# Performance work log

Hardware: AMD Instinct MI355X
Metric: run time of the kernel (lower is better)

The kernel has to match this reference:

```python
import jax, jax.numpy as jnp
import numpy as np

N_NODES = 50000
N_EDGES = 800000
NFEAT, NHID, NCLASS = 512, 64, 40


def setup_inputs() -> dict:
    key = jax.random.key(0)
    ks = jax.random.split(key, 10)
    x = jax.random.normal(ks[0], (N_NODES, NFEAT), dtype=jnp.float32)
    edge_weight = jax.random.uniform(ks[1], (N_EDGES,), dtype=jnp.float32)
    W1 = jax.random.normal(ks[2], (NFEAT, NHID), dtype=jnp.float32) / np.sqrt(NFEAT)
    b1 = jnp.zeros((NHID,), dtype=jnp.float32)
    W2 = jax.random.normal(ks[3], (NHID, NHID), dtype=jnp.float32) / np.sqrt(NHID)
    b2 = jnp.zeros((NHID,), dtype=jnp.float32)
    W3 = jax.random.normal(ks[4], (NHID, NCLASS), dtype=jnp.float32) / np.sqrt(NHID)
    b3 = jnp.zeros((NCLASS,), dtype=jnp.float32)
    row = jax.random.randint(ks[5], (N_EDGES,), 0, N_NODES, dtype=jnp.int32)
    col = jax.random.randint(ks[6], (N_EDGES,), 0, N_NODES, dtype=jnp.int32)
    return {"x": x, "edge_weight": edge_weight, "W1": W1, "b1": b1,
            "W2": W2, "b2": b2, "W3": W3, "b3": b3, "row": row, "col": col}


def _gcn_layer(h, W, b, row, col, ew):
    # support = h @ W + b ; out = spmm(adj, support)
    support = h @ W + b                      # [N, dout]
    msg = support[col] * ew[:, None]         # gather + scale, [E, dout]
    return jax.ops.segment_sum(msg, row, num_segments=N_NODES)


def reference(x, edge_weight, W1, b1, W2, b2, W3, b3, row, col):
    h = jax.nn.relu(_gcn_layer(x, W1, b1, row, col, edge_weight))
    # dropout: eval mode -> identity
    h = _gcn_layer(h, W2, b2, row, col, edge_weight)
    h = _gcn_layer(h, W3, b3, row, col, edge_weight)
    return jax.nn.log_softmax(h, axis=1)
```

## Files before the change

kernel.cpp:

```cpp
#include <hip/hip_runtime.h>
#include <hip/hip_bf16.h>

#define NNODES 50000
#define NEDGES 800000
#define NFEAT  512
#define NHID   64
#define NCLASS 40

#define CAP 48
#define CNTSTRIDE 16
#define EPT 4
#define FILL_CHUNKS ((NEDGES / EPT + 255) / 256)
#define GEMM1_BLOCKS ((NNODES + 31) / 32)
#define SPMM_BLOCKS ((NNODES + 15) / 16)

typedef __attribute__((ext_vector_type(8))) short short8;
typedef __attribute__((ext_vector_type(4))) float floatx4;

static __device__ __forceinline__ unsigned short f2bf(float f) {
    union { float f; unsigned u; } v; v.f = f;
    const unsigned r = v.u + 0x7fffu + ((v.u >> 16) & 1u);
    return (unsigned short)(r >> 16);
}
static __device__ __forceinline__ float bf2f(unsigned u) {
    union { unsigned u; float f; } v; v.u = u << 16;
    return v.f;
}

template<int NCB, int NVALID>
static __device__ __forceinline__ void convW_body(
    const float* __restrict__ W, unsigned short* __restrict__ wb, int idx) {
    const int lane = idx & 63;
    const int cb   = (idx >> 6) % NCB;
    const int kb   = idx / (64 * NCB);
    const int q = lane >> 4, m = lane & 15;
    const int c = cb * 16 + m;
    short8 v;
    #pragma unroll
    for (int j = 0; j < 8; ++j)
        v[j] = (c < NVALID)
             ? (short)f2bf(W[(size_t)(kb * 32 + q * 8 + j) * NVALID + c])
             : (short)0;
    *(short8*)(wb + (size_t)idx * 8) = v;
}

__global__ __launch_bounds__(256) void conv_kernel(
    const float* __restrict__ W1, unsigned short* __restrict__ wb1,
    const float* __restrict__ W2, unsigned short* __restrict__ wb2,
    const float* __restrict__ W3, unsigned short* __restrict__ wb3,
    int4* __restrict__ cnt4) {
    const int blk = blockIdx.x;
    const int tid = threadIdx.x;
    if (blk < 16) {
        convW_body<4, 64>(W1, wb1, blk * 256 + tid);
    } else if (blk < 18) {
        convW_body<4, 64>(W2, wb2, (blk - 16) * 256 + tid);
    } else if (blk < 20) {
        const int idx = (blk - 18) * 256 + tid;
        if (idx < 2 * 3 * 64) convW_body<3, 40>(W3, wb3, idx);
    } else {
        const int i = (blk - 20) * 256 + tid;
        if (i < NNODES * CNTSTRIDE / 4) cnt4[i] = make_int4(0, 0, 0, 0);
    }
}

__global__ __launch_bounds__(256) void bucket_gemm1_kernel(
    const int* __restrict__ row, const int* __restrict__ col,
    const float* __restrict__ ew, int* __restrict__ cnt,
    unsigned* __restrict__ bucket,
    const float* __restrict__ x, const unsigned short* __restrict__ wb,
    const float* __restrict__ b, unsigned short* __restrict__ outb) {
    const int blk  = blockIdx.x;
    const int tid  = threadIdx.x;
    const int base = blk / 3;
    const int r    = blk % 3;

    if (r == 2) {
        const int e = (base * 256 + tid) * EPT;
        if (e >= NEDGES) return;
        const int4   r4 = *(const int4*)(row + e);
        const int4   c4 = *(const int4*)(col + e);
        const float4 w4 = *(const float4*)(ew + e);
        const int p0 = atomicAdd(&cnt[r4.x * CNTSTRIDE], 1);
        const int p1 = atomicAdd(&cnt[r4.y * CNTSTRIDE], 1);
        const int p2 = atomicAdd(&cnt[r4.z * CNTSTRIDE], 1);
        const int p3 = atomicAdd(&cnt[r4.w * CNTSTRIDE], 1);
        if (p0 < CAP) bucket[(size_t)r4.x * CAP + p0] = (unsigned)c4.x | ((unsigned)f2bf(w4.x) << 16);
        if (p1 < CAP) bucket[(size_t)r4.y * CAP + p1] = (unsigned)c4.y | ((unsigned)f2bf(w4.y) << 16);
        if (p2 < CAP) bucket[(size_t)r4.z * CAP + p2] = (unsigned)c4.z | ((unsigned)f2bf(w4.z) << 16);
        if (p3 < CAP) bucket[(size_t)r4.w * CAP + p3] = (unsigned)c4.w | ((unsigned)f2bf(w4.w) << 16);
        return;
    }

    const int g = base * 2 + r;
    if (g >= GEMM1_BLOCKS) return;
    __shared__ float red[2][16][64];

    const int lane = tid & 63;
    const int wid  = tid >> 6;
    const int p  = wid >> 1;
    const int kh = wid & 1;
    const int q = lane >> 4, m = lane & 15;

    const int rowbase = g * 32 + p * 16;
    int rload = rowbase + m;
    if (rload >= NNODES) rload = NNODES - 1;
    const float* xp = x + (size_t)rload * NFEAT + kh * 256 + q * 8;

    floatx4 acc[4];
    #pragma unroll
    for (int cb = 0; cb < 4; ++cb) acc[cb] = (floatx4)0.f;

    #pragma unroll
    for (int kc = 0; kc < 2; ++kc) {
        float4 a0[4], a1[4];
        #pragma unroll
        for (int u = 0; u < 4; ++u) {
            a0[u] = *(const float4*)(xp + (kc * 4 + u) * 32);
            a1[u] = *(const float4*)(xp + (kc * 4 + u) * 32 + 4);
        }
        #pragma unroll
        for (int u = 0; u < 4; ++u) {
            short8 afrag;
            afrag[0] = (short)f2bf(a0[u].x); afrag[1] = (short)f2bf(a0[u].y);
            afrag[2] = (short)f2bf(a0[u].z); afrag[3] = (short)f2bf(a0[u].w);
            afrag[4] = (short)f2bf(a1[u].x); afrag[5] = (short)f2bf(a1[u].y);
            afrag[6] = (short)f2bf(a1[u].z); afrag[7] = (short)f2bf(a1[u].w);

            const int kbg = kh * 8 + kc * 4 + u;
            const unsigned short* wp = wb + ((size_t)(kbg * 4) * 64 + lane) * 8;
            #pragma unroll
            for (int cb = 0; cb < 4; ++cb) {
                const short8 bfrag = *(const short8*)(wp + (size_t)cb * 64 * 8);
                acc[cb] = __builtin_amdgcn_mfma_f32_16x16x32_bf16(
                    afrag, bfrag, acc[cb], 0, 0, 0);
            }
        }
    }

    if (kh == 1) {
        #pragma unroll
        for (int cb = 0; cb < 4; ++cb)
            #pragma unroll
            for (int i = 0; i < 4; ++i)
                red[p][q * 4 + i][cb * 16 + m] = acc[cb][i];
    }
    __syncthreads();
    if (kh == 1) return;

    const int orow = rowbase + q * 4;
    #pragma unroll
    for (int cb = 0; cb < 4; ++cb) {
        const int c = cb * 16 + m;
        const float bias = b[c];
        #pragma unroll
        for (int i = 0; i < 4; ++i) {
            const int rr2 = orow + i;
            if (rr2 < NNODES)
                outb[(size_t)rr2 * NHID + c] =
                    f2bf(acc[cb][i] + red[p][q * 4 + i][c] + bias);
        }
    }
}

template<bool RELU, int NCB, int NOUT>
__global__ __launch_bounds__(256) void spmm_gemm_kernel(
    const unsigned short* __restrict__ supb, const unsigned* __restrict__ bucket,
    const int* __restrict__ cnt, const unsigned short* __restrict__ wb,
    const float* __restrict__ bias, unsigned short* __restrict__ outb) {
    __shared__ unsigned ent[16][CAP];
    __shared__ unsigned short ht[16 * 72];

    const int tid  = threadIdx.x;
    const int wid  = tid >> 6;
    const int lane = tid & 63;
    const int half = lane >> 5;
    const int fp   = lane & 31;
    const int nb0  = blockIdx.x * 16;

    #pragma unroll
    for (int s = 0; s < 3; ++s) {
        const int idx = s * 256 + tid;
        const int ln  = idx / CAP;
        const int sl  = idx - ln * CAP;
        const int n   = nb0 + ln;
        int d = cnt[n * CNTSTRIDE];
        if (d > CAP) d = CAP;
        ent[ln][sl] = (sl < d) ? bucket[(size_t)n * CAP + sl] : 0u;
    }
    __syncthreads();

    const int lnb = wid * 4;
    float a0[4] = {0.f, 0.f, 0.f, 0.f}, a1[4] = {0.f, 0.f, 0.f, 0.f};
    int maxd = 0;
    #pragma unroll
    for (int jn = 0; jn < 4; ++jn) {
        int d = cnt[(nb0 + lnb + jn) * CNTSTRIDE];
        if (d > CAP) d = CAP;
        maxd = max(maxd, d);
    }

    for (int i = half; i < maxd; i += 8) {
        unsigned eb[4][4], vb[4][4];
        #pragma unroll
        for (int jn = 0; jn < 4; ++jn)
            #pragma unroll
            for (int j = 0; j < 4; ++j)
                eb[jn][j] = ent[lnb + jn][i + 2 * j];
        #pragma unroll
        for (int jn = 0; jn < 4; ++jn)
            #pragma unroll
            for (int j = 0; j < 4; ++j)
                vb[jn][j] = *(const unsigned*)(supb + (size_t)(eb[jn][j] & 0xffffu) * NHID + fp * 2);
        #pragma unroll
        for (int jn = 0; jn < 4; ++jn)
            #pragma unroll
            for (int j = 0; j < 4; ++j) {
                const float w = bf2f(eb[jn][j] >> 16);
                a0[jn] += w * bf2f(vb[jn][j] & 0xffffu);
                a1[jn] += w * bf2f(vb[jn][j] >> 16);
            }
    }
    #pragma unroll
    for (int jn = 0; jn < 4; ++jn) {
        a0[jn] += __shfl_xor(a0[jn], 32);
        a1[jn] += __shfl_xor(a1[jn], 32);
        if (RELU) { a0[jn] = fmaxf(a0[jn], 0.f); a1[jn] = fmaxf(a1[jn], 0.f); }
    }
    if (half == 0) {
        #pragma unroll
        for (int jn = 0; jn < 4; ++jn)
            *(unsigned*)&ht[(lnb + jn) * 72 + fp * 2] =
                (unsigned)f2bf(a0[jn]) | ((unsigned)f2bf(a1[jn]) << 16);
    }
    __syncthreads();

    if (wid != 0) return;
    const int q = lane >> 4, m = lane & 15;
    const unsigned short* hp = &ht[m * 72 + q * 8];

    floatx4 acc[NCB];
    #pragma unroll
    for (int cb = 0; cb < NCB; ++cb) acc[cb] = (floatx4)0.f;

    #pragma unroll
    for (int kb = 0; kb < 2; ++kb) {
        const short8 afrag = *(const short8*)(hp + kb * 32);
        const unsigned short* wp = wb + ((size_t)(kb * NCB) * 64 + lane) * 8;
        #pragma unroll
        for (int cb = 0; cb < NCB; ++cb) {
            const short8 bfrag = *(const short8*)(wp + (size_t)cb * 64 * 8);
            acc[cb] = __builtin_amdgcn_mfma_f32_16x16x32_bf16(
                afrag, bfrag, acc[cb], 0, 0, 0);
        }
    }

    const int rbase = nb0 + q * 4;
    #pragma unroll
    for (int cb = 0; cb < NCB; ++cb) {
        const int c = cb * 16 + m;
        if (c >= NOUT) continue;
        const float bv = bias[c];
        #pragma unroll
        for (int i = 0; i < 4; ++i)
            outb[(size_t)(rbase + i) * NOUT + c] = f2bf(acc[cb][i] + bv);
    }
}

__global__ __launch_bounds__(256) void spmm_bf40_lsm_kernel(
    const unsigned short* __restrict__ supb, const unsigned* __restrict__ bucket,
    const int* __restrict__ cnt, float* __restrict__ out) {
    __shared__ unsigned ent[16][CAP];

    const int tid = threadIdx.x;
    const int f   = tid & 63;
    const int wid = tid >> 6;
    const int nb0 = blockIdx.x * 16;

    #pragma unroll
    for (int s = 0; s < 3; ++s) {
        const int idx = s * 256 + tid;
        const int ln  = idx / CAP;
        const int sl  = idx - ln * CAP;
        const int n   = nb0 + ln;
        int d = cnt[n * CNTSTRIDE];
        if (d > CAP) d = CAP;
        ent[ln][sl] = (sl < d) ? bucket[(size_t)n * CAP + sl] : 0u;
    }
    __syncthreads();

    #pragma unroll
    for (int t = 0; t < 4; ++t) {
        const int ln = wid * 4 + t;
        const int n  = nb0 + ln;
        int deg = cnt[n * CNTSTRIDE];
        if (deg > CAP) deg = CAP;
        float acc = 0.f;
        if (f < NCLASS) {
            for (int i = 0; i < deg; i += 16) {
                unsigned eb[16]; float vb[16];
                #pragma unroll
                for (int j = 0; j < 16; ++j)
                    eb[j] = ent[ln][min(i + j, CAP - 1)];
                #pragma unroll
                for (int j = 0; j < 16; ++j)
                    vb[j] = bf2f(supb[(size_t)(eb[j] & 0xffffu) * NCLASS + f]);
                #pragma unroll
                for (int j = 0; j < 16; ++j)
                    acc += vb[j] * bf2f(eb[j] >> 16);
            }
        }
        float m = (f < NCLASS) ? acc : -1e30f;
        #pragma unroll
        for (int o = 32; o > 0; o >>= 1) m = fmaxf(m, __shfl_xor(m, o));
        float ex = (f < NCLASS) ? __expf(acc - m) : 0.f;
        #pragma unroll
        for (int o = 32; o > 0; o >>= 1) ex += __shfl_xor(ex, o);
        const float ls = __logf(ex) + m;
        if (f < NCLASS) out[(size_t)n * NCLASS + f] = acc - ls;
    }
}

extern "C" void kernel_launch(void* const* d_in, const int* in_sizes, int n_in,
                              void* d_out, int out_size, void* d_ws, size_t ws_size,
                              hipStream_t stream) {
    const float* x  = (const float*)d_in[0];
    const float* ew = (const float*)d_in[1];
    const float* W1 = (const float*)d_in[2];
    const float* b1 = (const float*)d_in[3];
    const float* W2 = (const float*)d_in[4];
    const float* b2 = (const float*)d_in[5];
    const float* W3 = (const float*)d_in[6];
    const float* b3 = (const float*)d_in[7];
    const int* row  = (const int*)d_in[8];
    const int* col  = (const int*)d_in[9];
    float* out = (float*)d_out;

    const size_t n64 = (size_t)NNODES * NHID;
    const size_t n40 = (size_t)NNODES * NCLASS;
    unsigned* bucket = (unsigned*)d_ws;
    int* cnt = (int*)(bucket + (size_t)NNODES * CAP);
    unsigned short* S1 = (unsigned short*)(cnt + (size_t)NNODES * CNTSTRIDE);
    unsigned short* S2 = S1 + n64;
    unsigned short* S3 = S2 + n64;
    unsigned short* wb1 = S3 + n40;
    unsigned short* wb2 = wb1 + 16 * 4 * 64 * 8;
    unsigned short* wb3 = wb2 + 2 * 4 * 64 * 8;

    conv_kernel<<<820, 256, 0, stream>>>(W1, wb1, W2, wb2, W3, wb3, (int4*)cnt);

    bucket_gemm1_kernel<<<3 * FILL_CHUNKS, 256, 0, stream>>>(
        row, col, ew, cnt, bucket, x, wb1, b1, S1);

    spmm_gemm_kernel<true, 4, 64><<<SPMM_BLOCKS, 256, 0, stream>>>(
        S1, bucket, cnt, wb2, b2, S2);

    spmm_gemm_kernel<false, 3, 40><<<SPMM_BLOCKS, 256, 0, stream>>>(
        S2, bucket, cnt, wb3, b3, S3);

    spmm_bf40_lsm_kernel<<<SPMM_BLOCKS, 256, 0, stream>>>(S3, bucket, cnt, out);
}
```

Before: 269.0 us.

## Replicate intermediate feature tables per XCC to localize SpMM gathers

Each layer's bf16 support table is written up to 8 times, one copy per XCC, as far as the workspace size allows. SpMM kernels read the XCC id from a hardware register and gather from their own replica. The aim is for each XCC's L2 to cache its own copy of the gathered rows, so random gathers hit local cache instead of crossing dies. The cost is several times more write traffic and workspace use for the intermediate outputs.

```diff
diff --git a/kernel.cpp b/kernel.cpp
--- a/kernel.cpp
+++ b/kernel.cpp
@@ -25,6 +25,12 @@
 static __device__ __forceinline__ float bf2f(unsigned u) {
     union { unsigned u; float f; } v; v.u = u << 16;
     return v.f;
+}
+
+static __device__ __forceinline__ int xcc_id() {
+    unsigned x;
+    asm volatile("s_getreg_b32 %0, hwreg(20, 0, 8)" : "=s"(x));
+    return (int)(x & 7u);
 }
 
 template<int NCB, int NVALID>
@@ -69,7 +75,8 @@
     const float* __restrict__ ew, int* __restrict__ cnt,
     unsigned* __restrict__ bucket,
     const float* __restrict__ x, const unsigned short* __restrict__ wb,
-    const float* __restrict__ b, unsigned short* __restrict__ outb) {
+    const float* __restrict__ b, unsigned short* __restrict__ outb,
+    int nrep, size_t outRep) {
     const int blk  = blockIdx.x;
     const int tid  = threadIdx.x;
     const int base = blk / 3;
@@ -156,9 +163,12 @@
         #pragma unroll
         for (int i = 0; i < 4; ++i) {
             const int rr2 = orow + i;
-            if (rr2 < NNODES)
-                outb[(size_t)rr2 * NHID + c] =
+            if (rr2 < NNODES) {
+                const unsigned short val =
                     f2bf(acc[cb][i] + red[p][q * 4 + i][c] + bias);
+                for (int rp = 0; rp < nrep; ++rp)
+                    outb[(size_t)rp * outRep + (size_t)rr2 * NHID + c] = val;
+            }
         }
     }
 }
@@ -167,7 +177,8 @@
 __global__ __launch_bounds__(256) void spmm_gemm_kernel(
     const unsigned short* __restrict__ supb, const unsigned* __restrict__ bucket,
     const int* __restrict__ cnt, const unsigned short* __restrict__ wb,
-    const float* __restrict__ bias, unsigned short* __restrict__ outb) {
+    const float* __restrict__ bias, unsigned short* __restrict__ outb,
+    int nrep, size_t inRep, size_t outRep) {
     __shared__ unsigned ent[16][CAP];
     __shared__ unsigned short ht[16 * 72];
 
@@ -177,6 +188,7 @@
     const int half = lane >> 5;
     const int fp   = lane & 31;
     const int nb0  = blockIdx.x * 16;
+    const unsigned short* sup = supb + (size_t)(xcc_id() & (nrep - 1)) * inRep;
 
     #pragma unroll
     for (int s = 0; s < 3; ++s) {
@@ -211,7 +223,7 @@
         for (int jn = 0; jn < 4; ++jn)
             #pragma unroll
             for (int j = 0; j < 4; ++j)
-                vb[jn][j] = *(const unsigned*)(supb + (size_t)(eb[jn][j] & 0xffffu) * NHID + fp * 2);
+                vb[jn][j] = *(const unsigned*)(sup + (size_t)(eb[jn][j] & 0xffffu) * NHID + fp * 2);
         #pragma unroll
         for (int jn = 0; jn < 4; ++jn)
             #pragma unroll
@@ -262,20 +274,25 @@
         if (c >= NOUT) continue;
         const float bv = bias[c];
         #pragma unroll
-        for (int i = 0; i < 4; ++i)
-            outb[(size_t)(rbase + i) * NOUT + c] = f2bf(acc[cb][i] + bv);
+        for (int i = 0; i < 4; ++i) {
+            const unsigned short v = f2bf(acc[cb][i] + bv);
+            for (int rp = 0; rp < nrep; ++rp)
+                outb[(size_t)rp * outRep + (size_t)(rbase + i) * NOUT + c] = v;
+        }
     }
 }
 
 __global__ __launch_bounds__(256) void spmm_bf40_lsm_kernel(
     const unsigned short* __restrict__ supb, const unsigned* __restrict__ bucket,
-    const int* __restrict__ cnt, float* __restrict__ out) {
+    const int* __restrict__ cnt, float* __restrict__ out,
+    int nrep, size_t inRep) {
     __shared__ unsigned ent[16][CAP];
 
     const int tid = threadIdx.x;
     const int f   = tid & 63;
     const int wid = tid >> 6;
     const int nb0 = blockIdx.x * 16;
+    const unsigned short* sup = supb + (size_t)(xcc_id() & (nrep - 1)) * inRep;
 
     #pragma unroll
     for (int s = 0; s < 3; ++s) {
@@ -304,7 +321,7 @@
                     eb[j] = ent[ln][min(i + j, CAP - 1)];
                 #pragma unroll
                 for (int j = 0; j < 16; ++j)
-                    vb[j] = bf2f(supb[(size_t)(eb[j] & 0xffffu) * NCLASS + f]);
+                    vb[j] = bf2f(sup[(size_t)(eb[j] & 0xffffu) * NCLASS + f]);
                 #pragma unroll
                 for (int j = 0; j < 16; ++j)
                     acc += vb[j] * bf2f(eb[j] >> 16);
@@ -338,25 +355,35 @@
 
     const size_t n64 = (size_t)NNODES * NHID;
     const size_t n40 = (size_t)NNODES * NCLASS;
+    const size_t nWb = (16 + 2) * 4 * 64 * 8 + 2 * 3 * 64 * 8;
+    int nrep = 8;
+    while (nrep > 1) {
+        const size_t bytes = (size_t)NNODES * CAP * 4 + (size_t)NNODES * CNTSTRIDE * 4
+                           + (size_t)nrep * (2 * n64 + n40) * 2 + nWb * 2;
+        if (bytes <= ws_size) break;
+        nrep >>= 1;
+    }
+
     unsigned* bucket = (unsigned*)d_ws;
     int* cnt = (int*)(bucket + (size_t)NNODES * CAP);
     unsigned short* S1 = (unsigned short*)(cnt + (size_t)NNODES * CNTSTRIDE);
-    unsigned short* S2 = S1 + n64;
-    unsigned short* S3 = S2 + n64;
-    unsigned short* wb1 = S3 + n40;
+    unsigned short* S2 = S1 + (size_t)nrep * n64;
+    unsigned short* S3 = S2 + (size_t)nrep * n64;
+    unsigned short* wb1 = S3 + (size_t)nrep * n40;
     unsigned short* wb2 = wb1 + 16 * 4 * 64 * 8;
     unsigned short* wb3 = wb2 + 2 * 4 * 64 * 8;
 
     conv_kernel<<<820, 256, 0, stream>>>(W1, wb1, W2, wb2, W3, wb3, (int4*)cnt);
 
     bucket_gemm1_kernel<<<3 * FILL_CHUNKS, 256, 0, stream>>>(
-        row, col, ew, cnt, bucket, x, wb1, b1, S1);
+        row, col, ew, cnt, bucket, x, wb1, b1, S1, nrep, n64);
 
     spmm_gemm_kernel<true, 4, 64><<<SPMM_BLOCKS, 256, 0, stream>>>(
-        S1, bucket, cnt, wb2, b2, S2);
+        S1, bucket, cnt, wb2, b2, S2, nrep, n64, n64);
 
     spmm_gemm_kernel<false, 3, 40><<<SPMM_BLOCKS, 256, 0, stream>>>(
-        S2, bucket, cnt, wb3, b3, S3);
-
-    spmm_bf40_lsm_kernel<<<SPMM_BLOCKS, 256, 0, stream>>>(S3, bucket, cnt, out);
-}
+        S2, bucket, cnt, wb3, b3, S3, nrep, n64, n40);
+
+    spmm_bf40_lsm_kernel<<<SPMM_BLOCKS, 256, 0, stream>>>(
+        S3, bucket, cnt, out, nrep, n40);
+}
```

Result: slower. 329.6 us (+22.5%).
